# Performance work log

Hardware: AMD Instinct MI355X
Metric: run time of the kernel (lower is better)

The kernel has to match this reference:

```python
import jax, jax.numpy as jnp
import numpy as np

# Model constants (match init_kwargs + mamba_ssm defaults)
CIN, COUT, K, STRIDE = 64, 128, 4, 4
D = 128            # d_model = features_out
DI = 256           # d_inner = 2*D (expand=2)
NSTATE = 16        # d_state
DCONV = 4          # depthwise conv width
DT_RANK = 8        # ceil(D/16)
NB = 3             # blocks per direction
NTOT = 2 * NB      # forward + backward stacks


def setup_inputs() -> dict:
    key = jax.random.key(0)
    ks = jax.random.split(key, 10)
    s = 0.02
    x = jax.random.normal(ks[0], (2, CIN, 8192), jnp.float32)
    convd_w = jax.random.normal(ks[1], (COUT, CIN, K), jnp.float32) * s
    convd_b = jnp.zeros((COUT,), jnp.float32)
    ln_w = jnp.ones((NTOT, D), jnp.float32)
    ln_b = jnp.zeros((NTOT, D), jnp.float32)
    in_proj_w = jax.random.normal(ks[2], (NTOT, 2 * DI, D), jnp.float32) * s
    conv_w = jax.random.normal(ks[3], (NTOT, DI, DCONV), jnp.float32) * s
    conv_b = jnp.zeros((NTOT, DI), jnp.float32)
    xproj_w = jax.random.normal(ks[4], (NTOT, DT_RANK + 2 * NSTATE, DI), jnp.float32) * s
    dtproj_w = jax.random.normal(ks[5], (NTOT, DI, DT_RANK), jnp.float32) * s
    dtproj_b = jax.random.normal(ks[6], (NTOT, DI), jnp.float32) * s
    # S4D-real init: A = -[1..N]
    A_log = jnp.log(jnp.broadcast_to(jnp.arange(1, NSTATE + 1, dtype=jnp.float32), (NTOT, DI, NSTATE)))
    Dparam = jnp.ones((NTOT, DI), jnp.float32)
    outproj_w = jax.random.normal(ks[7], (NTOT, D, DI), jnp.float32) * s
    return dict(x=x, convd_w=convd_w, convd_b=convd_b, ln_w=ln_w, ln_b=ln_b,
                in_proj_w=in_proj_w, conv_w=conv_w, conv_b=conv_b, xproj_w=xproj_w,
                dtproj_w=dtproj_w, dtproj_b=dtproj_b, A_log=A_log, Dparam=Dparam,
                outproj_w=outproj_w)


def _silu(x):
    return x * jax.nn.sigmoid(x)


def _layernorm(x, w, b, eps=1e-5):
    m = x.mean(-1, keepdims=True)
    xc = x - m
    v = (xc * xc).mean(-1, keepdims=True)
    return xc * jax.lax.rsqrt(v + eps) * w + b


def _mamba_mixer(x, in_proj_w, conv_w, conv_b, xproj_w, dtproj_w, dtproj_b, A_log, Dp, outproj_w):
    # x: (B, L, D)
    B, L, _ = x.shape
    xz = jnp.einsum('bld,ed->ble', x, in_proj_w)          # (B, L, 2*DI)
    xm, z = jnp.split(xz, 2, axis=-1)
    # causal depthwise conv (pad left DCONV-1, truncate to L)
    xp = jnp.pad(xm, ((0, 0), (DCONV - 1, 0), (0, 0)))
    xc = conv_b
    acc = jnp.zeros_like(xm)
    for k in range(DCONV):
        acc = acc + xp[:, k:k + L, :] * conv_w[:, k]
    xc = _silu(acc + conv_b)                               # (B, L, DI)
    dbc = jnp.einsum('ble,ne->bln', xc, xproj_w)           # (B, L, DT_RANK + 2N)
    dt, Bc, Cc = jnp.split(dbc, [DT_RANK, DT_RANK + NSTATE], axis=-1)
    dt = jax.nn.softplus(jnp.einsum('blr,dr->bld', dt, dtproj_w) + dtproj_b)  # (B, L, DI)
    A = -jnp.exp(A_log)                                    # (DI, N)
    dA = jnp.exp(dt[..., None] * A)                        # (B, L, DI, N)
    dBx = dt[..., None] * Bc[:, :, None, :] * xc[..., None]

    def step(h, inp):
        dA_t, dBx_t, C_t = inp
        h = dA_t * h + dBx_t                               # (B, DI, N)
        y = jnp.einsum('bdn,bn->bd', h, C_t)
        return h, y

    h0 = jnp.zeros((B, DI, NSTATE), x.dtype)
    _, ys = jax.lax.scan(step, h0, (jnp.swapaxes(dA, 0, 1), jnp.swapaxes(dBx, 0, 1), jnp.swapaxes(Cc, 0, 1)))
    y = jnp.swapaxes(ys, 0, 1)                             # (B, L, DI)
    y = (y + Dp * xc) * _silu(z)
    return jnp.einsum('ble,de->bld', y, outproj_w)         # (B, L, D)


def _mamba_stack(x, off, ln_w, ln_b, in_proj_w, conv_w, conv_b, xproj_w, dtproj_w, dtproj_b, A_log, Dparam, outproj_w):
    # mamba_ssm Block semantics: residual = x (+ prev residual); x = mixer(norm(residual))
    res = None
    cur = x
    for i in range(NB):
        j = off + i
        res = cur if res is None else cur + res
        hn = _layernorm(res, ln_w[j], ln_b[j])
        cur = _mamba_mixer(hn, in_proj_w[j], conv_w[j], conv_b[j], xproj_w[j],
                           dtproj_w[j], dtproj_b[j], A_log[j], Dparam[j], outproj_w[j])
    return cur, res


def reference(x, convd_w, convd_b, ln_w, ln_b, in_proj_w, conv_w, conv_b, xproj_w,
              dtproj_w, dtproj_b, A_log, Dparam, outproj_w):
    # downsampling conv + SiLU
    y = jax.lax.conv_general_dilated(x, convd_w, (STRIDE,), 'VALID',
                                     dimension_numbers=('NCH', 'OIH', 'NCH'))
    y = _silu(y + convd_b[None, :, None])                  # (B, COUT, L')
    h = jnp.swapaxes(y, 1, 2)                              # (B, L', D)
    xf, rf = _mamba_stack(h, 0, ln_w, ln_b, in_proj_w, conv_w, conv_b, xproj_w,
                          dtproj_w, dtproj_b, A_log, Dparam, outproj_w)
    xb, rb = _mamba_stack(h[:, ::-1, :], NB, ln_w, ln_b, in_proj_w, conv_w, conv_b, xproj_w,
                          dtproj_w, dtproj_b, A_log, Dparam, outproj_w)
    out = (xf + rf) + (xb + rb)[:, ::-1, :]
    return jnp.swapaxes(out, 1, 2), rf, rb
```

## Files before the change

kernel.cpp:

```cpp
#include <hip/hip_runtime.h>
#include <hip/hip_bf16.h>
#include <math.h>

#define B    2
#define CIN  64
#define LIN  8192
#define L    2048
#define D    128
#define DI   256
#define NS   16
#define RK   8
#define NSTREAM 4
#define CH   32
#define NCH  (L/CH)
#define TOK  (NSTREAM*L)
#define SZ_D ((size_t)TOK*D)
#define SZ_DI ((size_t)TOK*DI)
#define SXM 280
#define SHN 152

typedef short  bfrag __attribute__((ext_vector_type(8)));
typedef float  facc  __attribute__((ext_vector_type(4)));
#define MFMA __builtin_amdgcn_mfma_f32_16x16x32_bf16

__device__ __forceinline__ float sigmoidf_(float x){ return 1.f/(1.f+__expf(-x)); }
__device__ __forceinline__ float siluf_(float x){ return x*sigmoidf_(x); }
__device__ __forceinline__ ushort f2bf(float f){
    unsigned u = __float_as_uint(f);
    u += 0x7fffu + ((u>>16)&1u);
    return (ushort)(u>>16);
}
__device__ __forceinline__ float bf2f(ushort u){ return __uint_as_float(((unsigned)u)<<16); }
__device__ __forceinline__ float softplusf_(float t){
    return (t > 20.f) ? t : __logf(1.f + __expf(t));
}

__global__ void k_cvtall(const float* __restrict__ cw, const float* __restrict__ ipw,
                         const float* __restrict__ opw, const float* __restrict__ xpw,
                         ushort* __restrict__ dst){
    int i = blockIdx.x*256 + threadIdx.x;
    ushort v;
    if (i < 32768)       v = f2bf(cw[i]);
    else if (i < 425984) v = f2bf(ipw[i-32768]);
    else if (i < 622592) v = f2bf(opw[i-425984]);
    else {
        int t = i - 622592;
        int k = t & 255, nr = (t>>8) & 63, j = t>>14;
        v = (nr < 40) ? f2bf(xpw[((size_t)j*40 + nr)*256 + k]) : (ushort)0;
    }
    dst[i] = v;
}

__global__ void k_down(const float* __restrict__ x, const ushort* __restrict__ wd,
                       const float* __restrict__ bias, float* __restrict__ h){
    __shared__ ushort sxd[64*SXM];
    int tid = threadIdx.x;
    int m0 = blockIdx.x*64;
    int b = m0 >> 11;
    int l0 = m0 & 2047;
    for (int idx = tid; idx < 64*64; idx += 256){
        int t = idx & 63, cc = idx >> 6;
        float4 v = *(const float4*)(x + ((size_t)(b*CIN + cc))*LIN + 4*(l0+t));
        ushort4 o; o.x=f2bf(v.x); o.y=f2bf(v.y); o.z=f2bf(v.z); o.w=f2bf(v.w);
        *(ushort4*)&sxd[t*SXM + cc*4] = o;
    }
    __syncthreads();
    int w = tid>>6, lane = tid&63, rw = w>>1, cw = w&1;
    int q = lane>>4, r = lane&15;
    int n0 = blockIdx.y*64 + cw*32;
    const ushort* b0p = wd + (size_t)(n0 + r)*256 + q*8;
    const ushort* b1p = b0p + (size_t)16*256;
    facc acc[2][2] = {};
    #pragma unroll
    for (int kb=0; kb<8; ++kb){
        bfrag a0 = *(bfrag*)&sxd[(rw*32 + r)*SXM + kb*32 + q*8];
        bfrag a1 = *(bfrag*)&sxd[(rw*32 + 16 + r)*SXM + kb*32 + q*8];
        bfrag b0 = *(const bfrag*)(b0p + kb*32);
        bfrag b1 = *(const bfrag*)(b1p + kb*32);
        acc[0][0] = MFMA(a0,b0,acc[0][0],0,0,0);
        acc[0][1] = MFMA(a0,b1,acc[0][1],0,0,0);
        acc[1][0] = MFMA(a1,b0,acc[1][0],0,0,0);
        acc[1][1] = MFMA(a1,b1,acc[1][1],0,0,0);
    }
    #pragma unroll
    for (int im=0; im<2; ++im)
    #pragma unroll
    for (int in=0; in<2; ++in){
        int col = n0 + in*16 + r;
        float bv = bias[col];
        #pragma unroll
        for (int r2=0; r2<4; ++r2){
            int row = m0 + rw*32 + im*16 + q*4 + r2;
            int bb = row >> 11, l = row & 2047;
            float v = siluf_(acc[im][in][r2] + bv);
            h[((size_t)(bb*L + l))*D + col] = v;
            h[((size_t)((2+bb)*L + (L-1-l)))*D + col] = v;
        }
    }
}

__global__ void __launch_bounds__(256,1)
k_head(const float* __restrict__ curIn, const float* __restrict__ resIn,
       float* __restrict__ resOut,
       const float* __restrict__ lnw, const float* __restrict__ lnb,
       const ushort* __restrict__ wbi, const ushort* __restrict__ wbx,
       const float* __restrict__ cw, const float* __restrict__ cb,
       const float* __restrict__ Wdt, const float* __restrict__ bdt,
       const float* __restrict__ A_log,
       float* __restrict__ z, float* __restrict__ xc,
       float* __restrict__ dtr, float* __restrict__ Bc, float* __restrict__ Cc,
       float* __restrict__ Aprod, float* __restrict__ Bend, int blk, int first){
    __shared__ ushort smHn[35*SHN];
    __shared__ ushort smXm[35*SXM];
    __shared__ ushort smXc[32*SXM];
    __shared__ float  smDbc[32*68];
    const int tid = threadIdx.x;
    const int bi = blockIdx.x;
    const int s = bi >> 6, c = bi & 63;
    const int j = (s>>1)*3 + blk;
    const int base_tok = s*L + c*CH;

    {
        int t = tid >> 3, g8 = tid & 7;
        size_t off = (size_t)(base_tok + t)*D + g8*16;
        float4 v[4];
        const float4* cp = (const float4*)(curIn + off);
        #pragma unroll
        for (int i=0;i<4;++i) v[i] = cp[i];
        if (!first){
            const float4* rp = (const float4*)(resIn + off);
            #pragma unroll
            for (int i=0;i<4;++i){ float4 rv=rp[i]; v[i].x+=rv.x; v[i].y+=rv.y; v[i].z+=rv.z; v[i].w+=rv.w; }
        }
        {
            float4* ro = (float4*)(resOut + off);
            #pragma unroll
            for (int i=0;i<4;++i) ro[i] = v[i];
        }
        float s1=0.f, s2=0.f;
        #pragma unroll
        for (int i=0;i<4;++i){
            s1 += v[i].x+v[i].y+v[i].z+v[i].w;
            s2 += v[i].x*v[i].x+v[i].y*v[i].y+v[i].z*v[i].z+v[i].w*v[i].w;
        }
        s1 += __shfl_xor(s1,1); s2 += __shfl_xor(s2,1);
        s1 += __shfl_xor(s1,2); s2 += __shfl_xor(s2,2);
        s1 += __shfl_xor(s1,4); s2 += __shfl_xor(s2,4);
        float mean = s1*(1.f/128.f);
        float var  = s2*(1.f/128.f) - mean*mean;
        float rstd = rsqrtf(var + 1e-5f);
        const float4* lwp = (const float4*)(lnw + j*D + g8*16);
        const float4* lbp = (const float4*)(lnb + j*D + g8*16);
        #pragma unroll
        for (int i=0;i<4;++i){
            float4 lw = lwp[i], lb = lbp[i];
            ushort4 o;
            o.x = f2bf((v[i].x-mean)*rstd*lw.x + lb.x);
            o.y = f2bf((v[i].y-mean)*rstd*lw.y + lb.y);
            o.z = f2bf((v[i].z-mean)*rstd*lw.z + lb.z);
            o.w = f2bf((v[i].w-mean)*rstd*lw.w + lb.w);
            *(ushort4*)&smHn[t*SHN + g8*16 + i*4] = o;
        }
    }
    if (c > 0 && tid < 24){
        int t = tid >> 3, g8 = tid & 7;
        size_t off = (size_t)(base_tok - 3 + t)*D + g8*16;
        float4 v[4];
        const float4* cp = (const float4*)(curIn + off);
        #pragma unroll
        for (int i=0;i<4;++i) v[i] = cp[i];
        if (!first){
            const float4* rp = (const float4*)(resIn + off);
            #pragma unroll
            for (int i=0;i<4;++i){ float4 rv=rp[i]; v[i].x+=rv.x; v[i].y+=rv.y; v[i].z+=rv.z; v[i].w+=rv.w; }
        }
        float s1=0.f, s2=0.f;
        #pragma unroll
        for (int i=0;i<4;++i){
            s1 += v[i].x+v[i].y+v[i].z+v[i].w;
            s2 += v[i].x*v[i].x+v[i].y*v[i].y+v[i].z*v[i].z+v[i].w*v[i].w;
        }
        s1 += __shfl_xor(s1,1); s2 += __shfl_xor(s2,1);
        s1 += __shfl_xor(s1,2); s2 += __shfl_xor(s2,2);
        s1 += __shfl_xor(s1,4); s2 += __shfl_xor(s2,4);
        float mean = s1*(1.f/128.f);
        float var  = s2*(1.f/128.f) - mean*mean;
        float rstd = rsqrtf(var + 1e-5f);
        const float4* lwp = (const float4*)(lnw + j*D + g8*16);
        const float4* lbp = (const float4*)(lnb + j*D + g8*16);
        #pragma unroll
        for (int i=0;i<4;++i){
            float4 lw = lwp[i], lb = lbp[i];
            ushort4 o;
            o.x = f2bf((v[i].x-mean)*rstd*lw.x + lb.x);
            o.y = f2bf((v[i].y-mean)*rstd*lw.y + lb.y);
            o.z = f2bf((v[i].z-mean)*rstd*lw.z + lb.z);
            o.w = f2bf((v[i].w-mean)*rstd*lw.w + lb.w);
            *(ushort4*)&smHn[(32+t)*SHN + g8*16 + i*4] = o;
        }
    }
    __syncthreads();

    {
        int w = tid>>6, lane = tid&63, q = lane>>4, r = lane&15;
        bfrag a[3][4];
        #pragma unroll
        for (int rt=0; rt<3; ++rt)
        #pragma unroll
        for (int kb=0; kb<4; ++kb)
            a[rt][kb] = *(bfrag*)&smHn[(rt*16 + r)*SHN + kb*32 + q*8];
        #pragma unroll
        for (int ct=0; ct<8; ++ct){
            int n0 = w*128 + ct*16;
            const ushort* bp = wbi + ((size_t)j*512 + n0 + r)*128 + q*8;
            facc a0 = {}, a1 = {}, a2 = {};
            #pragma unroll
            for (int kb=0; kb<4; ++kb){
                bfrag bv = *(const bfrag*)(bp + kb*32);
                a0 = MFMA(a[0][kb], bv, a0, 0,0,0);
                a1 = MFMA(a[1][kb], bv, a1, 0,0,0);
                a2 = MFMA(a[2][kb], bv, a2, 0,0,0);
            }
            int colL = n0 + r;
            if (colL < DI){
                #pragma unroll
                for (int r2=0;r2<4;++r2){
                    int rr = q*4 + r2;
                    smXm[rr*SXM + colL]      = f2bf(a0[r2]);
                    smXm[(16+rr)*SXM + colL] = f2bf(a1[r2]);
                    if (rr < 3) smXm[(32+rr)*SXM + colL] = f2bf(a2[r2]);
                }
            } else {
                int cz = colL - DI;
                #pragma unroll
                for (int r2=0;r2<4;++r2){
                    int rr = q*4 + r2;
                    z[(size_t)(base_tok + rr)*DI + cz]      = a0[r2];
                    z[(size_t)(base_tok + 16 + rr)*DI + cz] = a1[r2];
                }
            }
        }
    }
    __syncthreads();

    {
        const float* w4 = cw + ((size_t)j*DI + tid)*4;
        float cw0=w4[0], cw1=w4[1], cw2=w4[2], cw3=w4[3];
        float cbb = cb[j*DI + tid];
        float xm1=0.f, xm2=0.f, xm3=0.f;
        if (c > 0){
            xm3 = bf2f(smXm[32*SXM + tid]);
            xm2 = bf2f(smXm[33*SXM + tid]);
            xm1 = bf2f(smXm[34*SXM + tid]);
        }
        #pragma unroll 4
        for (int i=0;i<CH;++i){
            float x0 = bf2f(smXm[i*SXM + tid]);
            float v = siluf_(cbb + cw3*x0 + cw2*xm1 + cw1*xm2 + cw0*xm3);
            smXc[i*SXM + tid] = f2bf(v);
            xc[(size_t)(base_tok+i)*DI + tid] = v;
            xm3 = xm2; xm2 = xm1; xm1 = x0;
        }
    }
    __syncthreads();

    {
        int w = tid>>6, lane = tid&63, q = lane>>4, r = lane&15;
        facc a0 = {}, a1 = {};
        const ushort* bp = wbx + ((size_t)j*64 + w*16 + r)*256 + q*8;
        #pragma unroll
        for (int kb=0; kb<8; ++kb){
            bfrag av0 = *(bfrag*)&smXc[r*SXM + kb*32 + q*8];
            bfrag av1 = *(bfrag*)&smXc[(16+r)*SXM + kb*32 + q*8];
            bfrag bv  = *(const bfrag*)(bp + kb*32);
            a0 = MFMA(av0, bv, a0, 0,0,0);
            a1 = MFMA(av1, bv, a1, 0,0,0);
        }
        int col = w*16 + r;
        #pragma unroll
        for (int r2=0;r2<4;++r2){
            int rr = q*4 + r2;
            smDbc[rr*68 + col]      = a0[r2];
            smDbc[(16+rr)*68 + col] = a1[r2];
            int row0 = base_tok + rr, row1 = base_tok + 16 + rr;
            if      (col < 8){  dtr[(size_t)row0*RK + col] = a0[r2];      dtr[(size_t)row1*RK + col] = a1[r2]; }
            else if (col < 24){ Bc [(size_t)row0*NS + (col-8)] = a0[r2];  Bc [(size_t)row1*NS + (col-8)] = a1[r2]; }
            else if (col < 40){ Cc [(size_t)row0*NS + (col-24)] = a0[r2]; Cc [(size_t)row1*NS + (col-24)] = a1[r2]; }
        }
    }
    __syncthreads();

    {
        float A[NS], wv[RK];
        const float* ar = A_log + ((size_t)j*DI + tid)*NS;
        #pragma unroll
        for (int n=0;n<NS;++n) A[n] = -__expf(ar[n]);
        const float* wr = Wdt + ((size_t)j*DI + tid)*RK;
        #pragma unroll
        for (int r=0;r<RK;++r) wv[r] = wr[r];
        float bb2 = bdt[j*DI + tid];
        float ap[NS], hs[NS];
        #pragma unroll
        for (int n=0;n<NS;++n){ ap[n]=1.f; hs[n]=0.f; }
        #pragma unroll 4
        for (int l=0;l<CH;++l){
            float t = bb2;
            #pragma unroll
            for (int r=0;r<RK;++r) t += smDbc[l*68+r]*wv[r];
            float dtv = softplusf_(t);
            float xv  = bf2f(smXc[l*SXM + tid]);
            float dbx = dtv*xv;
            #pragma unroll
            for (int n=0;n<NS;++n){
                float dA = __expf(dtv*A[n]);
                ap[n] *= dA;
                hs[n] = dA*hs[n] + dbx*smDbc[l*68+8+n];
            }
        }
        size_t pb = (size_t)bi*4096 + tid;
        #pragma unroll
        for (int n=0;n<NS;++n){
            Aprod[pb + (size_t)n*256] = ap[n];
            Bend [pb + (size_t)n*256] = hs[n];
        }
    }
}

__global__ void k_scanmid(const float* __restrict__ Aprod, float* __restrict__ Bend){
    int tid = blockIdx.x*128 + threadIdx.x;
    int s = tid >> 12;
    int nd = tid & 4095;
    size_t base = (size_t)s*NCH*4096 + nd;
    float h = 0.f;
    for (int c0=0; c0<NCH; c0+=16){
        float a[16], b[16];
        #pragma unroll
        for (int i=0;i<16;++i){
            a[i] = Aprod[base + (size_t)(c0+i)*4096];
            b[i] = Bend [base + (size_t)(c0+i)*4096];
        }
        #pragma unroll
        for (int i=0;i<16;++i){
            Bend[base + (size_t)(c0+i)*4096] = h;
            h = a[i]*h + b[i];
        }
    }
}

__global__ void k_tail(const float* __restrict__ dtr, const float* __restrict__ xcv,
                       const float* __restrict__ Bc, const float* __restrict__ Cc,
                       const float* __restrict__ A_log,
                       const float* __restrict__ Wdt, const float* __restrict__ bdt,
                       const float* __restrict__ h0, const float* __restrict__ z,
                       const float* __restrict__ Dp, const ushort* __restrict__ wbo,
                       float* __restrict__ cur, int blk){
    int c = blockIdx.x, s = blockIdx.y; int j = (s>>1)*3 + blk;
    int d = threadIdx.x;
    __shared__ float sB[CH*NS], sC[CH*NS], sdtr[CH*RK];
    __shared__ ushort sg[CH*SXM];
    int base_tok = s*L + c*CH;
    sB[d] = Bc[(size_t)base_tok*NS + d];
    sB[256+d] = Bc[(size_t)base_tok*NS + 256 + d];
    sC[d] = Cc[(size_t)base_tok*NS + d];
    sC[256+d] = Cc[(size_t)base_tok*NS + 256 + d];
    sdtr[d] = dtr[(size_t)base_tok*RK + d];
    float A[NS], wv[RK];
    const float* ar = A_log + ((size_t)j*DI + d)*NS;
    #pragma unroll
    for (int n=0;n<NS;++n) A[n] = -__expf(ar[n]);
    const float* wr = Wdt + ((size_t)j*DI + d)*RK;
    #pragma unroll
    for (int r=0;r<RK;++r) wv[r] = wr[r];
    float bb = bdt[j*DI + d];
    float Dpd = Dp[j*DI + d];
    float hs[NS];
    size_t pb = (size_t)(s*NCH + c)*4096 + d;
    #pragma unroll
    for (int n=0;n<NS;++n) hs[n] = h0[pb + (size_t)n*256];
    __syncthreads();
    #pragma unroll 4
    for (int l=0;l<CH;++l){
        float t = bb;
        #pragma unroll
        for (int r=0;r<RK;++r) t += sdtr[l*RK+r]*wv[r];
        float dtv = softplusf_(t);
        float xv  = xcv[(size_t)(base_tok+l)*DI + d];
        float dbx = dtv*xv;
        float p = 0.f;
        #pragma unroll
        for (int n=0;n<NS;++n){
            float dA = __expf(dtv*A[n]);
            hs[n] = dA*hs[n] + dbx*sB[l*NS+n];
            p += hs[n]*sC[l*NS+n];
        }
        float zv = z[(size_t)(base_tok+l)*DI + d];
        sg[l*SXM + d] = f2bf((p + Dpd*xv)*siluf_(zv));
    }
    __syncthreads();
    int w = d>>6, lane = d&63, q = lane>>4, r = lane&15;
    facc acc[2][2] = {};
    const ushort* b0p = wbo + ((size_t)j*128 + w*32 + r)*256 + q*8;
    const ushort* b1p = b0p + 16*256;
    #pragma unroll
    for (int kb=0; kb<8; ++kb){
        bfrag av0 = *(bfrag*)&sg[r*SXM + kb*32 + q*8];
        bfrag av1 = *(bfrag*)&sg[(16+r)*SXM + kb*32 + q*8];
        bfrag bv0 = *(const bfrag*)(b0p + kb*32);
        bfrag bv1 = *(const bfrag*)(b1p + kb*32);
        acc[0][0] = MFMA(av0,bv0,acc[0][0],0,0,0);
        acc[0][1] = MFMA(av0,bv1,acc[0][1],0,0,0);
        acc[1][0] = MFMA(av1,bv0,acc[1][0],0,0,0);
        acc[1][1] = MFMA(av1,bv1,acc[1][1],0,0,0);
    }
    #pragma unroll
    for (int rt=0; rt<2; ++rt)
    #pragma unroll
    for (int ct=0; ct<2; ++ct){
        int col = w*32 + ct*16 + r;
        #pragma unroll
        for (int r2=0;r2<4;++r2){
            int row = base_tok + rt*16 + q*4 + r2;
            cur[(size_t)row*D + col] = acc[rt][ct][r2];
        }
    }
}

__global__ void k_final(const float* __restrict__ cur, const float* __restrict__ res,
                        float* __restrict__ out){
    int l = blockIdx.x, b = blockIdx.y, d = threadIdx.x;
    int tf = (b*L + l)*D + d;
    int tbk = ((2+b)*L + (L-1-l))*D + d;
    float f  = cur[tf] + res[tf];
    float bw = cur[tbk] + res[tbk];
    out[((size_t)(b*D + d))*L + l] = f + bw;
    out[(size_t)2*D*L + (size_t)(b*L + l)*D + d] = res[tf];
    out[(size_t)2*D*L + (size_t)((2+b)*L + l)*D + d] = res[((2+b)*L + l)*D + d];
}

extern "C" void kernel_launch(void* const* d_in, const int* in_sizes, int n_in,
                              void* d_out, int out_size, void* d_ws, size_t ws_size,
                              hipStream_t stream){
    const float* x         = (const float*)d_in[0];
    const float* convd_w   = (const float*)d_in[1];
    const float* convd_b   = (const float*)d_in[2];
    const float* ln_w      = (const float*)d_in[3];
    const float* ln_b      = (const float*)d_in[4];
    const float* in_proj_w = (const float*)d_in[5];
    const float* conv_w    = (const float*)d_in[6];
    const float* conv_b    = (const float*)d_in[7];
    const float* xproj_w   = (const float*)d_in[8];
    const float* dtproj_w  = (const float*)d_in[9];
    const float* dtproj_b  = (const float*)d_in[10];
    const float* A_log     = (const float*)d_in[11];
    const float* Dparam    = (const float*)d_in[12];
    const float* outproj_w = (const float*)d_in[13];

    float* ws = (float*)d_ws;
    float* h     = ws; ws += SZ_D;
    float* res0  = ws; ws += SZ_D;
    float* res1  = ws; ws += SZ_D;
    float* cur   = ws; ws += SZ_D;
    float* z     = ws; ws += SZ_DI;
    float* xc    = ws; ws += SZ_DI;
    float* Aprod = ws; ws += SZ_D;
    float* Bend  = ws; ws += SZ_D;
    float* dtr   = ws; ws += (size_t)TOK*RK;
    float* Bc    = ws; ws += (size_t)TOK*NS;
    float* Cc    = ws; ws += (size_t)TOK*NS;
    ushort* wall = (ushort*)ws;
    ushort* wbd  = wall;
    ushort* wbi  = wall + 32768;
    ushort* wbo  = wall + 425984;
    ushort* wbx  = wall + 622592;

    k_cvtall<<<2816, 256, 0, stream>>>(convd_w, in_proj_w, outproj_w, xproj_w, wall);
    k_down<<<dim3(64, 2), 256, 0, stream>>>(x, wbd, convd_b, h);

    float* resin[3]  = { nullptr, res0, res1 };
    float* resout[3] = { res0,    res1, res0 };
    for (int blk = 0; blk < 3; ++blk){
        const float* ci = (blk==0) ? h : cur;
        const float* ri = (blk==0) ? h : resin[blk];
        k_head<<<NSTREAM*NCH, 256, 0, stream>>>(ci, ri, resout[blk], ln_w, ln_b, wbi, wbx,
                                                conv_w, conv_b, dtproj_w, dtproj_b, A_log,
                                                z, xc, dtr, Bc, Cc, Aprod, Bend, blk, blk==0);
        k_scanmid<<<128, 128, 0, stream>>>(Aprod, Bend);
        k_tail<<<dim3(NCH, NSTREAM), 256, 0, stream>>>(dtr, xc, Bc, Cc, A_log,
                                                       dtproj_w, dtproj_b, Bend, z,
                                                       Dparam, wbo, cur, blk);
    }

    k_final<<<dim3(L, B), 128, 0, stream>>>(cur, res0, (float*)d_out);
}
```

Before: 256.2 us.

## Fuse weight conversion into downsample, drop scanmid, store z/xc as bf16

Merges the weight-conversion and downsampling-conv kernels into one launch: the conv weights are converted to bf16 in shared memory and the projection weights are converted by extra blocks. Removes the separate chunk-carry scan kernel, so each tail block recomputes its starting state by walking all preceding chunk summaries, which are now stored in a vectorised float4 layout. z and xc are stored as bf16 instead of fp32 to halve that traffic. This cuts four launches per run and saves memory bandwidth, at the cost of redundant serial prefix work in later chunks (up to 63 steps) and lower precision for z and xc.

```diff
diff --git a/kernel.cpp b/kernel.cpp
--- a/kernel.cpp
+++ b/kernel.cpp
@@ -1,5 +1,4 @@
 #include <hip/hip_runtime.h>
-#include <hip/hip_bf16.h>
 #include <math.h>
 
 #define B    2
@@ -35,27 +34,32 @@
     return (t > 20.f) ? t : __logf(1.f + __expf(t));
 }
 
-__global__ void k_cvtall(const float* __restrict__ cw, const float* __restrict__ ipw,
-                         const float* __restrict__ opw, const float* __restrict__ xpw,
-                         ushort* __restrict__ dst){
-    int i = blockIdx.x*256 + threadIdx.x;
-    ushort v;
-    if (i < 32768)       v = f2bf(cw[i]);
-    else if (i < 425984) v = f2bf(ipw[i-32768]);
-    else if (i < 622592) v = f2bf(opw[i-425984]);
-    else {
-        int t = i - 622592;
-        int k = t & 255, nr = (t>>8) & 63, j = t>>14;
-        v = (nr < 40) ? f2bf(xpw[((size_t)j*40 + nr)*256 + k]) : (ushort)0;
-    }
-    dst[i] = v;
-}
-
-__global__ void k_down(const float* __restrict__ x, const ushort* __restrict__ wd,
-                       const float* __restrict__ bias, float* __restrict__ h){
+__global__ void __launch_bounds__(256,1)
+k_downcvt(const float* __restrict__ x, const float* __restrict__ convd_w,
+          const float* __restrict__ bias,
+          const float* __restrict__ ipw, const float* __restrict__ opw,
+          const float* __restrict__ xpw,
+          float* __restrict__ h, ushort* __restrict__ wall){
+    int tid = threadIdx.x;
+    if (blockIdx.x >= 128){
+        int g = (blockIdx.x - 128)*256 + tid;
+        for (int i = g; i < 688128; i += 32768){
+            ushort v;
+            if (i < 393216)      v = f2bf(ipw[i]);
+            else if (i < 589824) v = f2bf(opw[i-393216]);
+            else {
+                int t = i - 589824;
+                int k = t & 255, nr = (t>>8) & 63, jj = t>>14;
+                v = (nr < 40) ? f2bf(xpw[((size_t)jj*40 + nr)*256 + k]) : (ushort)0;
+            }
+            wall[i] = v;
+        }
+        return;
+    }
     __shared__ ushort sxd[64*SXM];
-    int tid = threadIdx.x;
-    int m0 = blockIdx.x*64;
+    __shared__ ushort swt[64*SXM];
+    int mb = blockIdx.x & 63, nb = blockIdx.x >> 6;
+    int m0 = mb*64;
     int b = m0 >> 11;
     int l0 = m0 & 2047;
     for (int idx = tid; idx < 64*64; idx += 256){
@@ -64,19 +68,23 @@
         ushort4 o; o.x=f2bf(v.x); o.y=f2bf(v.y); o.z=f2bf(v.z); o.w=f2bf(v.w);
         *(ushort4*)&sxd[t*SXM + cc*4] = o;
     }
-    __syncthreads();
-    int w = tid>>6, lane = tid&63, rw = w>>1, cw = w&1;
+    for (int idx = tid; idx < 64*64; idx += 256){
+        int cl = idx >> 6, kq = idx & 63;
+        float4 v = *(const float4*)(convd_w + ((size_t)(nb*64 + cl))*256 + kq*4);
+        ushort4 o; o.x=f2bf(v.x); o.y=f2bf(v.y); o.z=f2bf(v.z); o.w=f2bf(v.w);
+        *(ushort4*)&swt[cl*SXM + kq*4] = o;
+    }
+    __syncthreads();
+    int w = tid>>6, lane = tid&63, rw = w>>1, cw_ = w&1;
     int q = lane>>4, r = lane&15;
-    int n0 = blockIdx.y*64 + cw*32;
-    const ushort* b0p = wd + (size_t)(n0 + r)*256 + q*8;
-    const ushort* b1p = b0p + (size_t)16*256;
+    int n0 = nb*64 + cw_*32;
     facc acc[2][2] = {};
     #pragma unroll
     for (int kb=0; kb<8; ++kb){
         bfrag a0 = *(bfrag*)&sxd[(rw*32 + r)*SXM + kb*32 + q*8];
         bfrag a1 = *(bfrag*)&sxd[(rw*32 + 16 + r)*SXM + kb*32 + q*8];
-        bfrag b0 = *(const bfrag*)(b0p + kb*32);
-        bfrag b1 = *(const bfrag*)(b1p + kb*32);
+        bfrag b0 = *(bfrag*)&swt[(cw_*32 + r)*SXM + kb*32 + q*8];
+        bfrag b1 = *(bfrag*)&swt[(cw_*32 + 16 + r)*SXM + kb*32 + q*8];
         acc[0][0] = MFMA(a0,b0,acc[0][0],0,0,0);
         acc[0][1] = MFMA(a0,b1,acc[0][1],0,0,0);
         acc[1][0] = MFMA(a1,b0,acc[1][0],0,0,0);
@@ -107,7 +115,7 @@
        const float* __restrict__ cw, const float* __restrict__ cb,
        const float* __restrict__ Wdt, const float* __restrict__ bdt,
        const float* __restrict__ A_log,
-       float* __restrict__ z, float* __restrict__ xc,
+       ushort* __restrict__ zh, ushort* __restrict__ xch,
        float* __restrict__ dtr, float* __restrict__ Bc, float* __restrict__ Cc,
        float* __restrict__ Aprod, float* __restrict__ Bend, int blk, int first){
     __shared__ ushort smHn[35*SHN];
@@ -235,8 +243,8 @@
                 #pragma unroll
                 for (int r2=0;r2<4;++r2){
                     int rr = q*4 + r2;
-                    z[(size_t)(base_tok + rr)*DI + cz]      = a0[r2];
-                    z[(size_t)(base_tok + 16 + rr)*DI + cz] = a1[r2];
+                    zh[(size_t)(base_tok + rr)*DI + cz]      = f2bf(a0[r2]);
+                    zh[(size_t)(base_tok + 16 + rr)*DI + cz] = f2bf(a1[r2]);
                 }
             }
         }
@@ -257,8 +265,9 @@
         for (int i=0;i<CH;++i){
             float x0 = bf2f(smXm[i*SXM + tid]);
             float v = siluf_(cbb + cw3*x0 + cw2*xm1 + cw1*xm2 + cw0*xm3);
-            smXc[i*SXM + tid] = f2bf(v);
-            xc[(size_t)(base_tok+i)*DI + tid] = v;
+            ushort vb = f2bf(v);
+            smXc[i*SXM + tid] = vb;
+            xch[(size_t)(base_tok+i)*DI + tid] = vb;
             xm3 = xm2; xm2 = xm1; xm1 = x0;
         }
     }
@@ -317,43 +326,27 @@
                 hs[n] = dA*hs[n] + dbx*smDbc[l*68+8+n];
             }
         }
-        size_t pb = (size_t)bi*4096 + tid;
-        #pragma unroll
-        for (int n=0;n<NS;++n){
-            Aprod[pb + (size_t)n*256] = ap[n];
-            Bend [pb + (size_t)n*256] = hs[n];
-        }
-    }
-}
-
-__global__ void k_scanmid(const float* __restrict__ Aprod, float* __restrict__ Bend){
-    int tid = blockIdx.x*128 + threadIdx.x;
-    int s = tid >> 12;
-    int nd = tid & 4095;
-    size_t base = (size_t)s*NCH*4096 + nd;
-    float h = 0.f;
-    for (int c0=0; c0<NCH; c0+=16){
-        float a[16], b[16];
-        #pragma unroll
-        for (int i=0;i<16;++i){
-            a[i] = Aprod[base + (size_t)(c0+i)*4096];
-            b[i] = Bend [base + (size_t)(c0+i)*4096];
-        }
-        #pragma unroll
-        for (int i=0;i<16;++i){
-            Bend[base + (size_t)(c0+i)*4096] = h;
-            h = a[i]*h + b[i];
-        }
-    }
-}
-
-__global__ void k_tail(const float* __restrict__ dtr, const float* __restrict__ xcv,
-                       const float* __restrict__ Bc, const float* __restrict__ Cc,
-                       const float* __restrict__ A_log,
-                       const float* __restrict__ Wdt, const float* __restrict__ bdt,
-                       const float* __restrict__ h0, const float* __restrict__ z,
-                       const float* __restrict__ Dp, const ushort* __restrict__ wbo,
-                       float* __restrict__ cur, int blk){
+        size_t pb = (size_t)bi*4096 + (size_t)tid*16;
+        #pragma unroll
+        for (int k4=0;k4<4;++k4){
+            float4 av, bv;
+            av.x=ap[k4*4+0]; av.y=ap[k4*4+1]; av.z=ap[k4*4+2]; av.w=ap[k4*4+3];
+            bv.x=hs[k4*4+0]; bv.y=hs[k4*4+1]; bv.z=hs[k4*4+2]; bv.w=hs[k4*4+3];
+            *(float4*)&Aprod[pb + k4*4] = av;
+            *(float4*)&Bend [pb + k4*4] = bv;
+        }
+    }
+}
+
+__global__ void __launch_bounds__(256,1)
+k_tail(const float* __restrict__ dtr, const ushort* __restrict__ xch,
+       const float* __restrict__ Bc, const float* __restrict__ Cc,
+       const float* __restrict__ A_log,
+       const float* __restrict__ Wdt, const float* __restrict__ bdt,
+       const float* __restrict__ Aprod, const float* __restrict__ Bend,
+       const ushort* __restrict__ zh,
+       const float* __restrict__ Dp, const ushort* __restrict__ wbo,
+       float* __restrict__ cur, int blk){
     int c = blockIdx.x, s = blockIdx.y; int j = (s>>1)*3 + blk;
     int d = threadIdx.x;
     __shared__ float sB[CH*NS], sC[CH*NS], sdtr[CH*RK];
@@ -374,9 +367,21 @@
     float bb = bdt[j*DI + d];
     float Dpd = Dp[j*DI + d];
     float hs[NS];
-    size_t pb = (size_t)(s*NCH + c)*4096 + d;
-    #pragma unroll
-    for (int n=0;n<NS;++n) hs[n] = h0[pb + (size_t)n*256];
+    #pragma unroll
+    for (int n=0;n<NS;++n) hs[n] = 0.f;
+    {
+        size_t sb = ((size_t)(s*NCH))*4096 + (size_t)d*16;
+        for (int ci=0; ci<c; ++ci){
+            const float4* apv = (const float4*)&Aprod[sb + (size_t)ci*4096];
+            const float4* bpv = (const float4*)&Bend [sb + (size_t)ci*4096];
+            float4 a0=apv[0], a1=apv[1], a2=apv[2], a3=apv[3];
+            float4 b0=bpv[0], b1=bpv[1], b2=bpv[2], b3=bpv[3];
+            hs[0]=a0.x*hs[0]+b0.x; hs[1]=a0.y*hs[1]+b0.y; hs[2]=a0.z*hs[2]+b0.z; hs[3]=a0.w*hs[3]+b0.w;
+            hs[4]=a1.x*hs[4]+b1.x; hs[5]=a1.y*hs[5]+b1.y; hs[6]=a1.z*hs[6]+b1.z; hs[7]=a1.w*hs[7]+b1.w;
+            hs[8]=a2.x*hs[8]+b2.x; hs[9]=a2.y*hs[9]+b2.y; hs[10]=a2.z*hs[10]+b2.z; hs[11]=a2.w*hs[11]+b2.w;
+            hs[12]=a3.x*hs[12]+b3.x; hs[13]=a3.y*hs[13]+b3.y; hs[14]=a3.z*hs[14]+b3.z; hs[15]=a3.w*hs[15]+b3.w;
+        }
+    }
     __syncthreads();
     #pragma unroll 4
     for (int l=0;l<CH;++l){
@@ -384,7 +389,7 @@
         #pragma unroll
         for (int r=0;r<RK;++r) t += sdtr[l*RK+r]*wv[r];
         float dtv = softplusf_(t);
-        float xv  = xcv[(size_t)(base_tok+l)*DI + d];
+        float xv  = bf2f(xch[(size_t)(base_tok+l)*DI + d]);
         float dbx = dtv*xv;
         float p = 0.f;
         #pragma unroll
@@ -393,7 +398,7 @@
             hs[n] = dA*hs[n] + dbx*sB[l*NS+n];
             p += hs[n]*sC[l*NS+n];
         }
-        float zv = z[(size_t)(base_tok+l)*DI + d];
+        float zv = bf2f(zh[(size_t)(base_tok+l)*DI + d]);
         sg[l*SXM + d] = f2bf((p + Dpd*xv)*siluf_(zv));
     }
     __syncthreads();
@@ -460,21 +465,20 @@
     float* res0  = ws; ws += SZ_D;
     float* res1  = ws; ws += SZ_D;
     float* cur   = ws; ws += SZ_D;
-    float* z     = ws; ws += SZ_DI;
-    float* xc    = ws; ws += SZ_DI;
+    ushort* zh   = (ushort*)ws; ws += SZ_DI/2;
+    ushort* xch  = (ushort*)ws; ws += SZ_DI/2;
     float* Aprod = ws; ws += SZ_D;
     float* Bend  = ws; ws += SZ_D;
     float* dtr   = ws; ws += (size_t)TOK*RK;
     float* Bc    = ws; ws += (size_t)TOK*NS;
     float* Cc    = ws; ws += (size_t)TOK*NS;
     ushort* wall = (ushort*)ws;
-    ushort* wbd  = wall;
-    ushort* wbi  = wall + 32768;
-    ushort* wbo  = wall + 425984;
-    ushort* wbx  = wall + 622592;
-
-    k_cvtall<<<2816, 256, 0, stream>>>(convd_w, in_proj_w, outproj_w, xproj_w, wall);
-    k_down<<<dim3(64, 2), 256, 0, stream>>>(x, wbd, convd_b, h);
+    ushort* wbi  = wall;
+    ushort* wbo  = wall + 393216;
+    ushort* wbx  = wall + 589824;
+
+    k_downcvt<<<256, 256, 0, stream>>>(x, convd_w, convd_b, in_proj_w, outproj_w,
+                                       xproj_w, h, wall);
 
     float* resin[3]  = { nullptr, res0, res1 };
     float* resout[3] = { res0,    res1, res0 };
@@ -483,10 +487,9 @@
         const float* ri = (blk==0) ? h : resin[blk];
         k_head<<<NSTREAM*NCH, 256, 0, stream>>>(ci, ri, resout[blk], ln_w, ln_b, wbi, wbx,
                                                 conv_w, conv_b, dtproj_w, dtproj_b, A_log,
-                                                z, xc, dtr, Bc, Cc, Aprod, Bend, blk, blk==0);
-        k_scanmid<<<128, 128, 0, stream>>>(Aprod, Bend);
-        k_tail<<<dim3(NCH, NSTREAM), 256, 0, stream>>>(dtr, xc, Bc, Cc, A_log,
-                                                       dtproj_w, dtproj_b, Bend, z,
+                                                zh, xch, dtr, Bc, Cc, Aprod, Bend, blk, blk==0);
+        k_tail<<<dim3(NCH, NSTREAM), 256, 0, stream>>>(dtr, xch, Bc, Cc, A_log,
+                                                       dtproj_w, dtproj_b, Aprod, Bend, zh,
                                                        Dparam, wbo, cur, blk);
     }
 
```

Measured after the change: 320.4 us. +25.1%, slower.
